# Optimization experiments

Measured on AMD Instinct MI355X. Metric: run time of the kernel, lower is better.

## Reference

```python
import jax, jax.numpy as jnp
import numpy as np

DEPTH = 10
NUM_TREES = 16
WIDTH = 2 ** (DEPTH - 1)  # 512
BATCH = 1024


def setup_inputs() -> dict:
    key = jax.random.key(0)
    x = jax.random.normal(key, (BATCH, NUM_TREES * DEPTH * WIDTH), dtype=jnp.float32)
    return {"x": x}


def reference(x):
    # logits: [B, T, depth, width]
    logits = jnp.reshape(x, (-1, NUM_TREES, DEPTH, WIDTH))
    sigmoids = jax.nn.sigmoid(logits)
    # trees_flat: [B, T, 1]
    trees_flat = jnp.ones_like(logits[:, :, 0:1, 0])
    trees = None
    for i in range(DEPTH):
        # pool level-i sigmoids into 2**i segments of size width / 2**i
        pool = jnp.reshape(sigmoids[:, :, i, :], (-1, NUM_TREES, 2 ** i, WIDTH // (2 ** i)))
        d1 = jnp.mean(pool, axis=3)                      # [B, T, 2**i]
        decisions = jnp.stack([1.0 - d1, d1], axis=3)    # [B, T, 2**i, 2]
        trees = trees_flat[:, :, :, None] * decisions    # [B, T, 2**i, 2]
        trees_flat = jnp.reshape(trees, (-1, NUM_TREES, 2 ** (i + 1)))
    probabilities = jnp.sum(trees, axis=2)               # [B, T, 2]
    return probabilities[:, :, 1]                        # [B, T]
```

## Files before the change

kernel.cpp:

```cpp
#include <hip/hip_runtime.h>
#include <math.h>


#define NUM_TREES 16
#define DEPTH     10
#define WIDTH     512
#define BATCH     1024

__device__ __forceinline__ float sigmoidf_fast(float x) {
    return __fdividef(1.0f, 1.0f + __expf(-x));
}

__device__ __forceinline__ float sum8_sigmoid(const float4& a, const float4& b) {
    return sigmoidf_fast(a.x) + sigmoidf_fast(a.y) + sigmoidf_fast(a.z) + sigmoidf_fast(a.w) +
           sigmoidf_fast(b.x) + sigmoidf_fast(b.y) + sigmoidf_fast(b.z) + sigmoidf_fast(b.w);
}

__global__ __launch_bounds__(256) void ndt_kernel(const float* __restrict__ x,
                                                  float* __restrict__ out) {
    const int wave_id = (blockIdx.x * blockDim.x + threadIdx.x) >> 6;
    const int lane = threadIdx.x & 63;
    const int b = wave_id >> 4;
    const int t = wave_id & 15;

    const float* base = x + (size_t)b * (NUM_TREES * DEPTH * WIDTH)
                          + (size_t)t * (DEPTH * WIDTH);
    const int e0 = lane * 8;

    float4 rs[6][2];
#pragma unroll
    for (int i = 0; i < 6; ++i) {
        const float4* p = (const float4*)(base + i * WIDTH + e0);
        rs[i][0] = p[0];
        rs[i][1] = p[1];
    }
    float S[6];
#pragma unroll
    for (int i = 0; i < 6; ++i) S[i] = sum8_sigmoid(rs[i][0], rs[i][1]);

    float4 rv[4][2];
#pragma unroll
    for (int i = 0; i < 4; ++i) {
        const float4* p = (const float4*)(base + (6 + i) * WIDTH + e0);
        rv[i][0] = p[0];
        rv[i][1] = p[1];
    }

    float v[8];
    {
        const float* q = (const float*)&rv[3][0];
#pragma unroll
        for (int k = 0; k < 8; ++k) v[k] = sigmoidf_fast(q[k]);
    }
    {
        const float* q = (const float*)&rv[2][0];
#pragma unroll
        for (int k = 0; k < 4; ++k) {
            float d = 0.5f * (sigmoidf_fast(q[2 * k]) + sigmoidf_fast(q[2 * k + 1]));
            v[k] = (1.0f - d) * v[2 * k] + d * v[2 * k + 1];
        }
    }
    {
        const float* q = (const float*)&rv[1][0];
#pragma unroll
        for (int k = 0; k < 2; ++k) {
            float d = 0.25f * (sigmoidf_fast(q[4 * k])     + sigmoidf_fast(q[4 * k + 1]) +
                               sigmoidf_fast(q[4 * k + 2]) + sigmoidf_fast(q[4 * k + 3]));
            v[k] = (1.0f - d) * v[2 * k] + d * v[2 * k + 1];
        }
    }
    float vv;
    {
        const float d = sum8_sigmoid(rv[0][0], rv[0][1]) * 0.125f;
        vv = (1.0f - d) * v[0] + d * v[1];
    }

#pragma unroll
    for (int step = 0; step < 6; ++step) {
        const int h = 1 << step;
        const int lvl = 5 - step;
#pragma unroll
        for (int i2 = 0; i2 <= lvl; ++i2) S[i2] += __shfl_xor(S[i2], h, 64);

        const float d = S[lvl] * (1.0f / (float)(16 << step));
        const float vo = __shfl_xor(vv, h, 64);
        const bool upper = ((lane >> step) & 1) != 0;
        const float v_even = upper ? vo : vv;
        const float v_odd  = upper ? vv : vo;
        vv = (1.0f - d) * v_even + d * v_odd;
    }

    if (lane == 0) out[wave_id] = vv;
}

extern "C" void kernel_launch(void* const* d_in, const int* in_sizes, int n_in,
                              void* d_out, int out_size, void* d_ws, size_t ws_size,
                              hipStream_t stream) {
    const float* x = (const float*)d_in[0];
    float* out = (float*)d_out;
    const int total_waves = BATCH * NUM_TREES;
    const int block = 256;
    const int grid = total_waves / (block / 64);
    ndt_kernel<<<grid, block, 0, stream>>>(x, out);
}
```

Before: 434.5 us.

## Use persistent waves with software-prefetch of next tree's upper levels

```diff
diff --git a/kernel.cpp b/kernel.cpp
--- a/kernel.cpp
+++ b/kernel.cpp
@@ -6,6 +6,10 @@
 #define DEPTH     10
 #define WIDTH     512
 #define BATCH     1024
+
+#define PAIRS_TOTAL (BATCH * NUM_TREES)
+#define WAVES_PERSIST 4096
+#define ITERS (PAIRS_TOTAL / WAVES_PERSIST)
 
 __device__ __forceinline__ float sigmoidf_fast(float x) {
     return __fdividef(1.0f, 1.0f + __expf(-x));
@@ -18,79 +22,94 @@
 
 __global__ __launch_bounds__(256) void ndt_kernel(const float* __restrict__ x,
                                                   float* __restrict__ out) {
-    const int wave_id = (blockIdx.x * blockDim.x + threadIdx.x) >> 6;
+    const int wave0 = (blockIdx.x * blockDim.x + threadIdx.x) >> 6;
     const int lane = threadIdx.x & 63;
-    const int b = wave_id >> 4;
-    const int t = wave_id & 15;
-
-    const float* base = x + (size_t)b * (NUM_TREES * DEPTH * WIDTH)
-                          + (size_t)t * (DEPTH * WIDTH);
     const int e0 = lane * 8;
 
     float4 rs[6][2];
+    {
+        const float* b0 = x + (size_t)wave0 * (DEPTH * WIDTH) + e0;
 #pragma unroll
-    for (int i = 0; i < 6; ++i) {
-        const float4* p = (const float4*)(base + i * WIDTH + e0);
-        rs[i][0] = p[0];
-        rs[i][1] = p[1];
-    }
-    float S[6];
-#pragma unroll
-    for (int i = 0; i < 6; ++i) S[i] = sum8_sigmoid(rs[i][0], rs[i][1]);
-
-    float4 rv[4][2];
-#pragma unroll
-    for (int i = 0; i < 4; ++i) {
-        const float4* p = (const float4*)(base + (6 + i) * WIDTH + e0);
-        rv[i][0] = p[0];
-        rv[i][1] = p[1];
-    }
-
-    float v[8];
-    {
-        const float* q = (const float*)&rv[3][0];
-#pragma unroll
-        for (int k = 0; k < 8; ++k) v[k] = sigmoidf_fast(q[k]);
-    }
-    {
-        const float* q = (const float*)&rv[2][0];
-#pragma unroll
-        for (int k = 0; k < 4; ++k) {
-            float d = 0.5f * (sigmoidf_fast(q[2 * k]) + sigmoidf_fast(q[2 * k + 1]));
-            v[k] = (1.0f - d) * v[2 * k] + d * v[2 * k + 1];
+        for (int i = 0; i < 6; ++i) {
+            const float4* p = (const float4*)(b0 + i * WIDTH);
+            rs[i][0] = p[0];
+            rs[i][1] = p[1];
         }
-    }
-    {
-        const float* q = (const float*)&rv[1][0];
-#pragma unroll
-        for (int k = 0; k < 2; ++k) {
-            float d = 0.25f * (sigmoidf_fast(q[4 * k])     + sigmoidf_fast(q[4 * k + 1]) +
-                               sigmoidf_fast(q[4 * k + 2]) + sigmoidf_fast(q[4 * k + 3]));
-            v[k] = (1.0f - d) * v[2 * k] + d * v[2 * k + 1];
-        }
-    }
-    float vv;
-    {
-        const float d = sum8_sigmoid(rv[0][0], rv[0][1]) * 0.125f;
-        vv = (1.0f - d) * v[0] + d * v[1];
     }
 
 #pragma unroll
-    for (int step = 0; step < 6; ++step) {
-        const int h = 1 << step;
-        const int lvl = 5 - step;
+    for (int k = 0; k < ITERS; ++k) {
+        const int pair = wave0 + k * WAVES_PERSIST;
+        const float* bcur = x + (size_t)pair * (DEPTH * WIDTH) + e0;
+
+        float4 rv[4][2];
 #pragma unroll
-        for (int i2 = 0; i2 <= lvl; ++i2) S[i2] += __shfl_xor(S[i2], h, 64);
+        for (int i = 0; i < 4; ++i) {
+            const float4* p = (const float4*)(bcur + (6 + i) * WIDTH);
+            rv[i][0] = p[0];
+            rv[i][1] = p[1];
+        }
 
-        const float d = S[lvl] * (1.0f / (float)(16 << step));
-        const float vo = __shfl_xor(vv, h, 64);
-        const bool upper = ((lane >> step) & 1) != 0;
-        const float v_even = upper ? vo : vv;
-        const float v_odd  = upper ? vv : vo;
-        vv = (1.0f - d) * v_even + d * v_odd;
+        float S[6];
+#pragma unroll
+        for (int i = 0; i < 6; ++i) S[i] = sum8_sigmoid(rs[i][0], rs[i][1]);
+
+        if (k + 1 < ITERS) {
+            const float* bn = x + (size_t)(pair + WAVES_PERSIST) * (DEPTH * WIDTH) + e0;
+#pragma unroll
+            for (int i = 0; i < 6; ++i) {
+                const float4* p = (const float4*)(bn + i * WIDTH);
+                rs[i][0] = p[0];
+                rs[i][1] = p[1];
+            }
+        }
+
+        float v[8];
+        {
+            const float* q = (const float*)&rv[3][0];
+#pragma unroll
+            for (int kk = 0; kk < 8; ++kk) v[kk] = sigmoidf_fast(q[kk]);
+        }
+        {
+            const float* q = (const float*)&rv[2][0];
+#pragma unroll
+            for (int kk = 0; kk < 4; ++kk) {
+                float d = 0.5f * (sigmoidf_fast(q[2 * kk]) + sigmoidf_fast(q[2 * kk + 1]));
+                v[kk] = (1.0f - d) * v[2 * kk] + d * v[2 * kk + 1];
+            }
+        }
+        {
+            const float* q = (const float*)&rv[1][0];
+#pragma unroll
+            for (int kk = 0; kk < 2; ++kk) {
+                float d = 0.25f * (sigmoidf_fast(q[4 * kk])     + sigmoidf_fast(q[4 * kk + 1]) +
+                                   sigmoidf_fast(q[4 * kk + 2]) + sigmoidf_fast(q[4 * kk + 3]));
+                v[kk] = (1.0f - d) * v[2 * kk] + d * v[2 * kk + 1];
+            }
+        }
+        float vv;
+        {
+            const float d = sum8_sigmoid(rv[0][0], rv[0][1]) * 0.125f;
+            vv = (1.0f - d) * v[0] + d * v[1];
+        }
+
+#pragma unroll
+        for (int step = 0; step < 6; ++step) {
+            const int h = 1 << step;
+            const int lvl = 5 - step;
+#pragma unroll
+            for (int i2 = 0; i2 <= lvl; ++i2) S[i2] += __shfl_xor(S[i2], h, 64);
+
+            const float d = S[lvl] * (1.0f / (float)(16 << step));
+            const float vo = __shfl_xor(vv, h, 64);
+            const bool upper = ((lane >> step) & 1) != 0;
+            const float v_even = upper ? vo : vv;
+            const float v_odd  = upper ? vv : vo;
+            vv = (1.0f - d) * v_even + d * v_odd;
+        }
+
+        if (lane == 0) out[pair] = vv;
     }
-
-    if (lane == 0) out[wave_id] = vv;
 }
 
 extern "C" void kernel_launch(void* const* d_in, const int* in_sizes, int n_in,
@@ -98,8 +117,7 @@
                               hipStream_t stream) {
     const float* x = (const float*)d_in[0];
     float* out = (float*)d_out;
-    const int total_waves = BATCH * NUM_TREES;
     const int block = 256;
-    const int grid = total_waves / (block / 64);
+    const int grid = WAVES_PERSIST / (block / 64);
     ndt_kernel<<<grid, block, 0, stream>>>(x, out);
 }
```

New measurement: 437.6 us. Within noise of the previous version (+0.7%).
